# Optimization experiments

Measured on AMD Instinct MI355X. Metric: run time of the kernel, lower is better.

The kernel has to match this reference:

```python
import jax, jax.numpy as jnp
import numpy as np

N_PARTICLES = 100000
STATE_DIM = 64          # 3 + 2*2 + 57
MSG_OUT = 64
HIDDEN = 32
N_EDGES = 1600000


def _init_linear(key, fan_in, fan_out):
    kw, kb = jax.random.split(key)
    bound = 1.0 / np.sqrt(fan_in)
    W = jax.random.uniform(kw, (fan_in, fan_out), minval=-bound, maxval=bound, dtype=jnp.float32)
    b = jax.random.uniform(kb, (fan_out,), minval=-bound, maxval=bound, dtype=jnp.float32)
    return W, b


def setup_inputs() -> dict:
    key = jax.random.key(0)
    ks = jax.random.split(key, 8)
    x = jax.random.normal(ks[0], (N_PARTICLES, STATE_DIM), dtype=jnp.float32)
    edge_index = jax.random.randint(ks[1], (2, N_EDGES), 0, N_PARTICLES, dtype=jnp.int64)
    # message conv MLP: [2*STATE_DIM] -> 32 -> 32 -> MSG_OUT
    mW1, mb1 = _init_linear(ks[2], 2 * STATE_DIM, HIDDEN)
    mW2, mb2 = _init_linear(ks[3], HIDDEN, HIDDEN)
    mW3, mb3 = _init_linear(ks[4], HIDDEN, MSG_OUT)
    # own_state_nn MLP: [STATE_DIM + MSG_OUT] -> 32 -> 32 -> STATE_DIM
    oW1, ob1 = _init_linear(ks[5], STATE_DIM + MSG_OUT, HIDDEN)
    oW2, ob2 = _init_linear(ks[6], HIDDEN, HIDDEN)
    oW3, ob3 = _init_linear(ks[7], HIDDEN, STATE_DIM)
    return {"x": x, "edge_index": edge_index,
            "mW1": mW1, "mb1": mb1, "mW2": mW2, "mb2": mb2, "mW3": mW3, "mb3": mb3,
            "oW1": oW1, "ob1": ob1, "oW2": oW2, "ob2": ob2, "oW3": oW3, "ob3": ob3}


def _mlp3(h, W1, b1, W2, b2, W3, b3):
    h = jax.nn.relu(h @ W1 + b1)
    h = jax.nn.relu(h @ W2 + b2)
    return h @ W3 + b3


def reference(x, edge_index, mW1, mb1, mW2, mb2, mW3, mb3,
              oW1, ob1, oW2, ob2, oW3, ob3):
    src, dst = edge_index[0], edge_index[1]
    # edge-wise message: MLP over [x_src || x_dst]  -> [E, MSG_OUT]
    e_feat = jnp.concatenate([x[src], x[dst]], axis=-1)  # [E, 2*STATE_DIM]
    m = _mlp3(e_feat, mW1, mb1, mW2, mb2, mW3, mb3)
    # scatter-sum aggregation at destination node
    messages = jax.ops.segment_sum(m, dst, num_segments=x.shape[0])  # [N, MSG_OUT]
    combined = jnp.concatenate([x, messages], axis=-1)  # [N, STATE_DIM+MSG_OUT]
    new_state = _mlp3(combined, oW1, ob1, oW2, ob2, oW3, ob3)
    return new_state
```

## Files before the change

### kernel.cpp

```cpp
#include <hip/hip_runtime.h>

#define NP 100000
#define NE 1600000
#define SD 64
#define HID 32
#define MSG 64
#define NP_PAD 100352
#define NTILE (NP / 16)
#define BINSZ 512
#define NBIN ((NP + BINSZ - 1) / BINSZ)
#define EPW 8192
#define NWG ((NE + EPW - 1) / EPW)

typedef float v4f __attribute__((ext_vector_type(4)));
typedef short v4s __attribute__((ext_vector_type(4)));
typedef short v8s __attribute__((ext_vector_type(8)));
typedef __bf16 v8bf __attribute__((ext_vector_type(8)));

#define WQ_FRAGS 56

__device__ __forceinline__ v4f MFMA32(v8s a, v8s b, v4f c) {
  return __builtin_amdgcn_mfma_f32_16x16x32_bf16(
      __builtin_bit_cast(v8bf, a), __builtin_bit_cast(v8bf, b), c, 0, 0, 0);
}

__device__ __forceinline__ short f2bf(float f) {
  return __builtin_bit_cast(short, (__bf16)f);
}
__device__ __forceinline__ float bf2f(short s) {
  unsigned u = ((unsigned)(unsigned short)s) << 16;
  return __builtin_bit_cast(float, u);
}

__device__ __forceinline__ v4f mfma3(v8s ah, v8s al, v8s bh, v8s bl, v4f c) {
  c = MFMA32(al, bh, c);
  c = MFMA32(ah, bl, c);
  c = MFMA32(ah, bh, c);
  return c;
}

__device__ __forceinline__ void load_wfrag(const float* __restrict__ W, int ld,
                                           int kb, int m0, int lq, int l15,
                                           v8s* hi, v8s* lo) {
  v8s h, l;
#pragma unroll
  for (int j = 0; j < 8; ++j) {
    int k = kb + ((j < 4) ? (4 * lq + j) : (16 + 4 * lq + (j - 4)));
    float v = W[k * ld + m0 + l15];
    short hb = f2bf(v);
    h[j] = hb;
    l[j] = f2bf(v - bf2f(hb));
  }
  *hi = h;
  *lo = l;
}

__device__ __forceinline__ void split8(v4f a, v4f b, v8s* hi, v8s* lo) {
  v8s h, l;
#pragma unroll
  for (int j = 0; j < 4; ++j) {
    short ha = f2bf(a[j]); h[j] = ha; l[j] = f2bf(a[j] - bf2f(ha));
    short hb = f2bf(b[j]); h[j + 4] = hb; l[j + 4] = f2bf(b[j] - bf2f(hb));
  }
  *hi = h;
  *lo = l;
}

__device__ __forceinline__ void load_xfrag(const float* xs, int kb, int lq,
                                           v8s* hi, v8s* lo) {
  v4f a = *reinterpret_cast<const v4f*>(xs + kb + 4 * lq);
  v4f b = *reinterpret_cast<const v4f*>(xs + kb + 16 + 4 * lq);
  split8(a, b, hi, lo);
}

__device__ __forceinline__ void chain_frag(v4f d0, v4f d1, v8s* hi, v8s* lo) {
  v4f a, b;
#pragma unroll
  for (int j = 0; j < 4; ++j) {
    a[j] = fmaxf(d0[j], 0.f);
    b[j] = fmaxf(d1[j], 0.f);
  }
  split8(a, b, hi, lo);
}


__global__ void prew_kernel(const float* __restrict__ mW1,
                            const float* __restrict__ mW2,
                            const float* __restrict__ mW3,
                            const float* __restrict__ oW1,
                            const float* __restrict__ oW2,
                            const float* __restrict__ oW3,
                            short* __restrict__ wqs) {
  int lane = threadIdx.x;
  int l15 = lane & 15, lq = lane >> 4;
  v8s* wq = reinterpret_cast<v8s*>(wqs);
  v8s h, l;
#pragma unroll
  for (int t = 0; t < 2; ++t)
#pragma unroll
    for (int kc = 0; kc < 2; ++kc) {
      load_wfrag(mW1, HID, kc * 32, t * 16, lq, l15, &h, &l);
      wq[(t * 2 + kc) * 64 + lane] = h;
      wq[(4 + t * 2 + kc) * 64 + lane] = l;
      load_wfrag(mW1, HID, 64 + kc * 32, t * 16, lq, l15, &h, &l);
      wq[(8 + t * 2 + kc) * 64 + lane] = h;
      wq[(12 + t * 2 + kc) * 64 + lane] = l;
    }
#pragma unroll
  for (int t = 0; t < 2; ++t) {
    load_wfrag(mW2, HID, 0, t * 16, lq, l15, &h, &l);
    wq[(16 + t) * 64 + lane] = h;
    wq[(18 + t) * 64 + lane] = l;
  }
#pragma unroll
  for (int t = 0; t < 4; ++t) {
    load_wfrag(mW3, MSG, 0, t * 16, lq, l15, &h, &l);
    wq[(20 + t) * 64 + lane] = h;
    wq[(24 + t) * 64 + lane] = l;
  }
#pragma unroll
  for (int t = 0; t < 2; ++t)
#pragma unroll
    for (int kc = 0; kc < 4; ++kc) {
      load_wfrag(oW1, HID, kc * 32, t * 16, lq, l15, &h, &l);
      wq[(28 + t * 4 + kc) * 64 + lane] = h;
      wq[(36 + t * 4 + kc) * 64 + lane] = l;
    }
#pragma unroll
  for (int t = 0; t < 2; ++t) {
    load_wfrag(oW2, HID, 0, t * 16, lq, l15, &h, &l);
    wq[(44 + t) * 64 + lane] = h;
    wq[(46 + t) * 64 + lane] = l;
  }
#pragma unroll
  for (int t = 0; t < 4; ++t) {
    load_wfrag(oW3, SD, 0, t * 16, lq, l15, &h, &l);
    wq[(48 + t) * 64 + lane] = h;
    wq[(52 + t) * 64 + lane] = l;
  }
}

__global__ __launch_bounds__(256, 2) void prep_kernel(
    const float* __restrict__ x, const short* __restrict__ wqs,
    const float* __restrict__ mb1,
    float* __restrict__ h1d_buf, short* __restrict__ h1s_buf) {
  const int lane = threadIdx.x & 63;
  const int l15 = lane & 15;
  const int lq = lane >> 4;
  const int tile = (blockIdx.x * 256 + threadIdx.x) >> 6;
  if (tile >= NTILE) return;
  const v8s* wq = reinterpret_cast<const v8s*>(wqs);

  const int node = tile * 16 + l15;
  v4f d0, d1, s0 = {0.f, 0.f, 0.f, 0.f}, s1 = {0.f, 0.f, 0.f, 0.f};
#pragma unroll
  for (int q = 0; q < 4; ++q) {
    d0[q] = mb1[4 * lq + q];
    d1[q] = mb1[16 + 4 * lq + q];
  }
#pragma unroll
  for (int kc = 0; kc < 2; ++kc) {
    v8s xh, xl;
    load_xfrag(x + (size_t)node * SD, kc * 32, lq, &xh, &xl);
    d0 = mfma3(wq[(8 + kc) * 64 + lane], wq[(12 + kc) * 64 + lane], xh, xl, d0);
    d1 = mfma3(wq[(10 + kc) * 64 + lane], wq[(14 + kc) * 64 + lane], xh, xl, d1);
    s0 = mfma3(wq[(0 + kc) * 64 + lane], wq[(4 + kc) * 64 + lane], xh, xl, s0);
    s1 = mfma3(wq[(2 + kc) * 64 + lane], wq[(6 + kc) * 64 + lane], xh, xl, s1);
  }
  *reinterpret_cast<v4f*>(h1d_buf + (size_t)node * HID + 4 * lq) = d0;
  *reinterpret_cast<v4f*>(h1d_buf + (size_t)node * HID + 16 + 4 * lq) = d1;
  v4s q0, q1;
#pragma unroll
  for (int q = 0; q < 4; ++q) {
    q0[q] = f2bf(s0[q]);
    q1[q] = f2bf(s1[q]);
  }
  *reinterpret_cast<v4s*>(h1s_buf + (size_t)node * HID + 4 * lq) = q0;
  *reinterpret_cast<v4s*>(h1s_buf + (size_t)node * HID + 16 + 4 * lq) = q1;
}


__global__ __launch_bounds__(256) void bin_count_kernel(
    const int* __restrict__ ei, int* __restrict__ gOff) {
  __shared__ int cnt[NBIN];
  const int w = blockIdx.x;
  for (int i = threadIdx.x; i < NBIN; i += 256) cnt[i] = 0;
  __syncthreads();
  const int e0 = w * EPW;
  const int e1 = (e0 + EPW < NE) ? e0 + EPW : NE;
  for (int e = e0 + threadIdx.x; e < e1; e += 256)
    atomicAdd(&cnt[ei[NE + e] >> 9], 1);
  __syncthreads();
  for (int i = threadIdx.x; i < NBIN; i += 256) gOff[i * NWG + w] = cnt[i];
}

__global__ __launch_bounds__(256) void scan_bins_kernel(
    int* __restrict__ gOff, int* __restrict__ binStart) {
  __shared__ int tot[NBIN];
  const int b = threadIdx.x;
  if (b < NBIN) {
    int run = 0;
    for (int w = 0; w < NWG; ++w) {
      int v = gOff[b * NWG + w];
      gOff[b * NWG + w] = run;
      run += v;
    }
    tot[b] = run;
  }
  __syncthreads();
  if (threadIdx.x == 0) {
    int run = 0;
    for (int bb = 0; bb < NBIN; ++bb) {
      binStart[bb] = run;
      run += tot[bb];
    }
    binStart[NBIN] = run;
  }
  __syncthreads();
  if (b < NBIN) {
    int base = binStart[b];
    for (int w = 0; w < NWG; ++w) gOff[b * NWG + w] += base;
  }
}

__global__ __launch_bounds__(256) void bin_scatter_kernel(
    const int* __restrict__ ei, const int* __restrict__ gOff,
    int2* __restrict__ pairs) {
  __shared__ int cur[NBIN];
  const int w = blockIdx.x;
  for (int i = threadIdx.x; i < NBIN; i += 256) cur[i] = gOff[i * NWG + w];
  __syncthreads();
  const int e0 = w * EPW;
  const int e1 = (e0 + EPW < NE) ? e0 + EPW : NE;
  for (int e = e0 + threadIdx.x; e < e1; e += 256) {
    int s = ei[e];
    int d = ei[NE + e];
    int pos = atomicAdd(&cur[d >> 9], 1);
    pairs[pos] = make_int2(s, d);
  }
}

__global__ __launch_bounds__(512) void bin_csr_kernel(
    const int2* __restrict__ pairs, const int* __restrict__ binStart,
    int2* __restrict__ co, int* __restrict__ csr_src) {
  __shared__ int sh[BINSZ];
  __shared__ int cu[BINSZ];
  const int b = blockIdx.x;
  const int t = threadIdx.x;
  cu[t] = 0;
  __syncthreads();
  const int p0 = binStart[b], p1 = binStart[b + 1];
  for (int p = p0 + t; p < p1; p += BINSZ)
    atomicAdd(&cu[pairs[p].y & (BINSZ - 1)], 1);
  __syncthreads();
  const int v = cu[t];
  sh[t] = v;
  __syncthreads();
  for (int off = 1; off < BINSZ; off <<= 1) {
    int a = (t >= off) ? sh[t - off] : 0;
    __syncthreads();
    sh[t] += a;
    __syncthreads();
  }
  const int excl = sh[t] - v;
  const int node = b * BINSZ + t;
  if (node < NP) co[node] = make_int2(p0 + excl, v);
  cu[t] = excl;
  __syncthreads();
  for (int p = p0 + t; p < p1; p += BINSZ) {
    int2 pr = pairs[p];
    int loc = atomicAdd(&cu[pr.y & (BINSZ - 1)], 1);
    csr_src[p0 + loc] = pr.x;
  }
}

__global__ __launch_bounds__(256, 4) void edge_mfma_kernel(
    const short* __restrict__ h1s, const float* __restrict__ h1d_buf,
    const short* __restrict__ wqs, const int2* __restrict__ co,
    const int* __restrict__ csr_src, const float* __restrict__ mb2,
    float* __restrict__ rsum) {
  const int lane = threadIdx.x & 63;
  const int l15 = lane & 15;
  const int lq = lane >> 4;
  const int wid = (blockIdx.x * 256 + threadIdx.x) >> 6;
  const int nw = gridDim.x * 4;
  const v8s* wq = reinterpret_cast<const v8s*>(wqs);

  const v8s w2h0 = wq[16 * 64 + lane], w2h1 = wq[17 * 64 + lane];
  const v8s w2l0 = wq[18 * 64 + lane], w2l1 = wq[19 * 64 + lane];
  v4f bb0, bb1;
#pragma unroll
  for (int q = 0; q < 4; ++q) {
    bb0[q] = mb2[4 * lq + q];
    bb1[q] = mb2[16 + 4 * lq + q];
  }

  for (int n = wid; n < NP; n += nw) {
    const int2 c = co[n];
    const int off = c.x, cnt = c.y;
    const int ng = (cnt + 15) >> 4;

    const v4f h1d0 = *reinterpret_cast<const v4f*>(h1d_buf + (size_t)n * HID + 4 * lq);
    const v4f h1d1 = *reinterpret_cast<const v4f*>(h1d_buf + (size_t)n * HID + 16 + 4 * lq);

    v4f r0 = {0.f, 0.f, 0.f, 0.f}, r1 = {0.f, 0.f, 0.f, 0.f};

    int rem = cnt;
    bool vcur = l15 < rem;
    int scur = vcur ? csr_src[off + l15] : 0;
    v4s ca = *reinterpret_cast<const v4s*>(h1s + (size_t)scur * HID + 4 * lq);
    v4s cb = *reinterpret_cast<const v4s*>(h1s + (size_t)scur * HID + 16 + 4 * lq);

    for (int g = 0; g < ng; ++g) {
      int rem2 = rem - 16;
      bool vnxt = l15 < rem2;
      int snxt = vnxt ? csr_src[off + (g + 1) * 16 + l15] : 0;
      v4s na = *reinterpret_cast<const v4s*>(h1s + (size_t)snxt * HID + 4 * lq);
      v4s nb = *reinterpret_cast<const v4s*>(h1s + (size_t)snxt * HID + 16 + 4 * lq);

      v4f d0, d1;
#pragma unroll
      for (int q = 0; q < 4; ++q) {
        d0[q] = h1d0[q] + bf2f(ca[q]);
        d1[q] = h1d1[q] + bf2f(cb[q]);
      }

      v8s ph, pl;
      chain_frag(d0, d1, &ph, &pl);
      v4f e0 = bb0, e1 = bb1;
      e0 = mfma3(w2h0, w2l0, ph, pl, e0);
      e1 = mfma3(w2h1, w2l1, ph, pl, e1);

      if (vcur) {
#pragma unroll
        for (int j = 0; j < 4; ++j) {
          r0[j] += fmaxf(e0[j], 0.f);
          r1[j] += fmaxf(e1[j], 0.f);
        }
      }
      ca = na;
      cb = nb;
      vcur = vnxt;
      rem = rem2;
    }

#pragma unroll
    for (int j = 0; j < 4; ++j) {
      float a = r0[j], b = r1[j];
      a += __shfl_xor(a, 1); a += __shfl_xor(a, 2);
      a += __shfl_xor(a, 4); a += __shfl_xor(a, 8);
      b += __shfl_xor(b, 1); b += __shfl_xor(b, 2);
      b += __shfl_xor(b, 4); b += __shfl_xor(b, 8);
      r0[j] = a; r1[j] = b;
    }
    if (l15 == 0) {
      *reinterpret_cast<v4f*>(rsum + (size_t)n * HID + 4 * lq) = r0;
      *reinterpret_cast<v4f*>(rsum + (size_t)n * HID + 16 + 4 * lq) = r1;
    }
  }
}

__global__ __launch_bounds__(256, 2) void fused_tail_kernel(
    const float* __restrict__ x, const short* __restrict__ wqs,
    const float* __restrict__ rsum, const int2* __restrict__ co,
    const float* __restrict__ mb3,
    const float* __restrict__ ob1, const float* __restrict__ ob2,
    const float* __restrict__ ob3,
    float* __restrict__ out) {
  const int lane = threadIdx.x & 63;
  const int l15 = lane & 15;
  const int lq = lane >> 4;
  const int tile = (blockIdx.x * 256 + threadIdx.x) >> 6;
  if (tile >= NTILE) return;
  const v8s* wq = reinterpret_cast<const v8s*>(wqs);

  const int node = tile * 16 + l15;
  const float fc = (float)co[node].y;

  v4f ra = *reinterpret_cast<const v4f*>(rsum + (size_t)node * HID + 4 * lq);
  v4f rb = *reinterpret_cast<const v4f*>(rsum + (size_t)node * HID + 16 + 4 * lq);
  v8s bh, bl;
  split8(ra, rb, &bh, &bl);

  v4f m[4];
#pragma unroll
  for (int t = 0; t < 4; ++t) {
    v4f c = {0.f, 0.f, 0.f, 0.f};
    c = mfma3(wq[(20 + t) * 64 + lane], wq[(24 + t) * 64 + lane], bh, bl, c);
#pragma unroll
    for (int q = 0; q < 4; ++q) c[q] += fc * mb3[t * 16 + 4 * lq + q];
    m[t] = c;
  }

  v4f d0, d1;
#pragma unroll
  for (int q = 0; q < 4; ++q) {
    d0[q] = ob1[4 * lq + q];
    d1[q] = ob1[16 + 4 * lq + q];
  }
#pragma unroll
  for (int kc = 0; kc < 2; ++kc) {
    v8s xh, xl;
    load_xfrag(x + (size_t)node * SD, kc * 32, lq, &xh, &xl);
    d0 = mfma3(wq[(28 + kc) * 64 + lane], wq[(36 + kc) * 64 + lane], xh, xl, d0);
    d1 = mfma3(wq[(32 + kc) * 64 + lane], wq[(40 + kc) * 64 + lane], xh, xl, d1);
  }
#pragma unroll
  for (int kc = 0; kc < 2; ++kc) {
    v8s mh, ml;
    split8(m[kc * 2], m[kc * 2 + 1], &mh, &ml);
    d0 = mfma3(wq[(30 + kc) * 64 + lane], wq[(38 + kc) * 64 + lane], mh, ml, d0);
    d1 = mfma3(wq[(34 + kc) * 64 + lane], wq[(42 + kc) * 64 + lane], mh, ml, d1);
  }

  v8s ph, pl;
  chain_frag(d0, d1, &ph, &pl);
  v4f e0, e1;
#pragma unroll
  for (int q = 0; q < 4; ++q) {
    e0[q] = ob2[4 * lq + q];
    e1[q] = ob2[16 + 4 * lq + q];
  }
  e0 = mfma3(wq[44 * 64 + lane], wq[46 * 64 + lane], ph, pl, e0);
  e1 = mfma3(wq[45 * 64 + lane], wq[47 * 64 + lane], ph, pl, e1);

  v8s rh, rl;
  chain_frag(e0, e1, &rh, &rl);
  float* orow = out + (size_t)node * SD;
#pragma unroll
  for (int t = 0; t < 4; ++t) {
    v4f c;
#pragma unroll
    for (int q = 0; q < 4; ++q) c[q] = ob3[t * 16 + 4 * lq + q];
    c = mfma3(wq[(48 + t) * 64 + lane], wq[(52 + t) * 64 + lane], rh, rl, c);
    *reinterpret_cast<v4f*>(orow + t * 16 + 4 * lq) = c;
  }
}

extern "C" void kernel_launch(void* const* d_in, const int* in_sizes, int n_in,
                              void* d_out, int out_size, void* d_ws,
                              size_t ws_size, hipStream_t stream) {
  const float* x = (const float*)d_in[0];
  const int* ei = (const int*)d_in[1];
  const float* mW1 = (const float*)d_in[2];
  const float* mb1 = (const float*)d_in[3];
  const float* mW2 = (const float*)d_in[4];
  const float* mb2 = (const float*)d_in[5];
  const float* mW3 = (const float*)d_in[6];
  const float* mb3 = (const float*)d_in[7];
  const float* oW1 = (const float*)d_in[8];
  const float* ob1 = (const float*)d_in[9];
  const float* oW2 = (const float*)d_in[10];
  const float* ob2 = (const float*)d_in[11];
  const float* oW3 = (const float*)d_in[12];
  const float* ob3 = (const float*)d_in[13];
  float* out = (float*)d_out;

  float* h1d_buf = (float*)d_out;
  short* h1s_buf = (short*)((char*)d_out + (size_t)NP * HID * 4);

  char* p = (char*)d_ws;
  short* wqs = (short*)p;            p += (size_t)WQ_FRAGS * 64 * 16;
  int* gOff = (int*)p;               p += (size_t)NBIN * NWG * 4;
  int* binStart = (int*)p;           p += 200 * 4;
  int2* co = (int2*)p;               p += (size_t)NP_PAD * 8;
  int* csr_src = (int*)p;            p += (size_t)NE * 4;
  int2* pairs = (int2*)p;
  float* rsum = (float*)pairs;

  prew_kernel<<<1, 64, 0, stream>>>(mW1, mW2, mW3, oW1, oW2, oW3, wqs);

  const int tile_blocks = (NTILE + 3) / 4;
  prep_kernel<<<tile_blocks, 256, 0, stream>>>(x, wqs, mb1, h1d_buf, h1s_buf);

  bin_count_kernel<<<NWG, 256, 0, stream>>>(ei, gOff);
  scan_bins_kernel<<<1, 256, 0, stream>>>(gOff, binStart);
  bin_scatter_kernel<<<NWG, 256, 0, stream>>>(ei, gOff, pairs);
  bin_csr_kernel<<<NBIN, 512, 0, stream>>>(pairs, binStart, co, csr_src);

  edge_mfma_kernel<<<2048, 256, 0, stream>>>(
      h1s_buf, h1d_buf, wqs, co, csr_src, mb2, rsum);

  fused_tail_kernel<<<tile_blocks, 256, 0, stream>>>(
      x, wqs, rsum, co, mb3, ob1, ob2, ob3, out);
}
```

Measured before the change: 173.4 us.

## Merge weight prep, node prep and bin count into one launch; deepen edge prefetch

Three small kernels (weight fragment packing, per-node first-layer precompute, destination bin counting) become one setup kernel whose blocks pick a role from blockIdx. This removes two launches and their serialization gaps. The node-prep blocks now read and split mW1 fragments directly instead of waiting on packed weights. Separately, the edge loop prefetches source features two groups ahead instead of one, to hide more gather latency at the cost of extra registers.

```diff
diff --git a/kernel.cpp b/kernel.cpp
--- a/kernel.cpp
+++ b/kernel.cpp
@@ -7,6 +7,7 @@
 #define MSG 64
 #define NP_PAD 100352
 #define NTILE (NP / 16)
+#define TILE_BLOCKS ((NTILE + 3) / 4)
 #define BINSZ 512
 #define NBIN ((NP + BINSZ - 1) / BINSZ)
 #define EPW 8192
@@ -83,75 +84,87 @@
   split8(a, b, hi, lo);
 }
 
-
-__global__ void prew_kernel(const float* __restrict__ mW1,
-                            const float* __restrict__ mW2,
-                            const float* __restrict__ mW3,
-                            const float* __restrict__ oW1,
-                            const float* __restrict__ oW2,
-                            const float* __restrict__ oW3,
-                            short* __restrict__ wqs) {
-  int lane = threadIdx.x;
-  int l15 = lane & 15, lq = lane >> 4;
-  v8s* wq = reinterpret_cast<v8s*>(wqs);
-  v8s h, l;
-#pragma unroll
-  for (int t = 0; t < 2; ++t)
-#pragma unroll
-    for (int kc = 0; kc < 2; ++kc) {
-      load_wfrag(mW1, HID, kc * 32, t * 16, lq, l15, &h, &l);
-      wq[(t * 2 + kc) * 64 + lane] = h;
-      wq[(4 + t * 2 + kc) * 64 + lane] = l;
-      load_wfrag(mW1, HID, 64 + kc * 32, t * 16, lq, l15, &h, &l);
-      wq[(8 + t * 2 + kc) * 64 + lane] = h;
-      wq[(12 + t * 2 + kc) * 64 + lane] = l;
-    }
-#pragma unroll
-  for (int t = 0; t < 2; ++t) {
-    load_wfrag(mW2, HID, 0, t * 16, lq, l15, &h, &l);
-    wq[(16 + t) * 64 + lane] = h;
-    wq[(18 + t) * 64 + lane] = l;
-  }
-#pragma unroll
-  for (int t = 0; t < 4; ++t) {
-    load_wfrag(mW3, MSG, 0, t * 16, lq, l15, &h, &l);
-    wq[(20 + t) * 64 + lane] = h;
-    wq[(24 + t) * 64 + lane] = l;
-  }
-#pragma unroll
-  for (int t = 0; t < 2; ++t)
-#pragma unroll
-    for (int kc = 0; kc < 4; ++kc) {
-      load_wfrag(oW1, HID, kc * 32, t * 16, lq, l15, &h, &l);
-      wq[(28 + t * 4 + kc) * 64 + lane] = h;
-      wq[(36 + t * 4 + kc) * 64 + lane] = l;
-    }
-#pragma unroll
-  for (int t = 0; t < 2; ++t) {
-    load_wfrag(oW2, HID, 0, t * 16, lq, l15, &h, &l);
-    wq[(44 + t) * 64 + lane] = h;
-    wq[(46 + t) * 64 + lane] = l;
-  }
-#pragma unroll
-  for (int t = 0; t < 4; ++t) {
-    load_wfrag(oW3, SD, 0, t * 16, lq, l15, &h, &l);
-    wq[(48 + t) * 64 + lane] = h;
-    wq[(52 + t) * 64 + lane] = l;
-  }
-}
-
-__global__ __launch_bounds__(256, 2) void prep_kernel(
-    const float* __restrict__ x, const short* __restrict__ wqs,
-    const float* __restrict__ mb1,
+__global__ __launch_bounds__(256, 2) void setup_kernel(
+    const float* __restrict__ x, const int* __restrict__ ei,
+    const float* __restrict__ mW1, const float* __restrict__ mb1,
+    const float* __restrict__ mW2, const float* __restrict__ mW3,
+    const float* __restrict__ oW1, const float* __restrict__ oW2,
+    const float* __restrict__ oW3,
+    int* __restrict__ gOff, short* __restrict__ wqs,
     float* __restrict__ h1d_buf, short* __restrict__ h1s_buf) {
+  __shared__ int cnt[NBIN];
+  const int blk = blockIdx.x;
+
+  if (blk < NWG) {
+    for (int i = threadIdx.x; i < NBIN; i += 256) cnt[i] = 0;
+    __syncthreads();
+    const int e0 = blk * EPW;
+    const int e1 = (e0 + EPW < NE) ? e0 + EPW : NE;
+    for (int e = e0 + threadIdx.x; e < e1; e += 256)
+      atomicAdd(&cnt[ei[NE + e] >> 9], 1);
+    __syncthreads();
+    for (int i = threadIdx.x; i < NBIN; i += 256) gOff[i * NWG + blk] = cnt[i];
+    return;
+  }
+
   const int lane = threadIdx.x & 63;
   const int l15 = lane & 15;
   const int lq = lane >> 4;
-  const int tile = (blockIdx.x * 256 + threadIdx.x) >> 6;
+
+  if (blk == NWG) {
+    if (threadIdx.x >= 64) return;
+    v8s* wq = reinterpret_cast<v8s*>(wqs);
+    v8s h, l;
+#pragma unroll
+    for (int t = 0; t < 2; ++t)
+#pragma unroll
+      for (int kc = 0; kc < 2; ++kc) {
+        load_wfrag(mW1, HID, kc * 32, t * 16, lq, l15, &h, &l);
+        wq[(t * 2 + kc) * 64 + lane] = h;
+        wq[(4 + t * 2 + kc) * 64 + lane] = l;
+        load_wfrag(mW1, HID, 64 + kc * 32, t * 16, lq, l15, &h, &l);
+        wq[(8 + t * 2 + kc) * 64 + lane] = h;
+        wq[(12 + t * 2 + kc) * 64 + lane] = l;
+      }
+#pragma unroll
+    for (int t = 0; t < 2; ++t) {
+      load_wfrag(mW2, HID, 0, t * 16, lq, l15, &h, &l);
+      wq[(16 + t) * 64 + lane] = h;
+      wq[(18 + t) * 64 + lane] = l;
+    }
+#pragma unroll
+    for (int t = 0; t < 4; ++t) {
+      load_wfrag(mW3, MSG, 0, t * 16, lq, l15, &h, &l);
+      wq[(20 + t) * 64 + lane] = h;
+      wq[(24 + t) * 64 + lane] = l;
+    }
+#pragma unroll
+    for (int t = 0; t < 2; ++t)
+#pragma unroll
+      for (int kc = 0; kc < 4; ++kc) {
+        load_wfrag(oW1, HID, kc * 32, t * 16, lq, l15, &h, &l);
+        wq[(28 + t * 4 + kc) * 64 + lane] = h;
+        wq[(36 + t * 4 + kc) * 64 + lane] = l;
+      }
+#pragma unroll
+    for (int t = 0; t < 2; ++t) {
+      load_wfrag(oW2, HID, 0, t * 16, lq, l15, &h, &l);
+      wq[(44 + t) * 64 + lane] = h;
+      wq[(46 + t) * 64 + lane] = l;
+    }
+#pragma unroll
+    for (int t = 0; t < 4; ++t) {
+      load_wfrag(oW3, SD, 0, t * 16, lq, l15, &h, &l);
+      wq[(48 + t) * 64 + lane] = h;
+      wq[(52 + t) * 64 + lane] = l;
+    }
+    return;
+  }
+
+  const int tile = ((blk - NWG - 1) * 256 + (int)threadIdx.x) >> 6;
   if (tile >= NTILE) return;
-  const v8s* wq = reinterpret_cast<const v8s*>(wqs);
-
   const int node = tile * 16 + l15;
+
   v4f d0, d1, s0 = {0.f, 0.f, 0.f, 0.f}, s1 = {0.f, 0.f, 0.f, 0.f};
 #pragma unroll
   for (int q = 0; q < 4; ++q) {
@@ -160,12 +173,16 @@
   }
 #pragma unroll
   for (int kc = 0; kc < 2; ++kc) {
-    v8s xh, xl;
+    v8s xh, xl, wh, wl;
     load_xfrag(x + (size_t)node * SD, kc * 32, lq, &xh, &xl);
-    d0 = mfma3(wq[(8 + kc) * 64 + lane], wq[(12 + kc) * 64 + lane], xh, xl, d0);
-    d1 = mfma3(wq[(10 + kc) * 64 + lane], wq[(14 + kc) * 64 + lane], xh, xl, d1);
-    s0 = mfma3(wq[(0 + kc) * 64 + lane], wq[(4 + kc) * 64 + lane], xh, xl, s0);
-    s1 = mfma3(wq[(2 + kc) * 64 + lane], wq[(6 + kc) * 64 + lane], xh, xl, s1);
+    load_wfrag(mW1, HID, 64 + kc * 32, 0, lq, l15, &wh, &wl);
+    d0 = mfma3(wh, wl, xh, xl, d0);
+    load_wfrag(mW1, HID, 64 + kc * 32, 16, lq, l15, &wh, &wl);
+    d1 = mfma3(wh, wl, xh, xl, d1);
+    load_wfrag(mW1, HID, kc * 32, 0, lq, l15, &wh, &wl);
+    s0 = mfma3(wh, wl, xh, xl, s0);
+    load_wfrag(mW1, HID, kc * 32, 16, lq, l15, &wh, &wl);
+    s1 = mfma3(wh, wl, xh, xl, s1);
   }
   *reinterpret_cast<v4f*>(h1d_buf + (size_t)node * HID + 4 * lq) = d0;
   *reinterpret_cast<v4f*>(h1d_buf + (size_t)node * HID + 16 + 4 * lq) = d1;
@@ -179,20 +196,6 @@
   *reinterpret_cast<v4s*>(h1s_buf + (size_t)node * HID + 16 + 4 * lq) = q1;
 }
 
-
-__global__ __launch_bounds__(256) void bin_count_kernel(
-    const int* __restrict__ ei, int* __restrict__ gOff) {
-  __shared__ int cnt[NBIN];
-  const int w = blockIdx.x;
-  for (int i = threadIdx.x; i < NBIN; i += 256) cnt[i] = 0;
-  __syncthreads();
-  const int e0 = w * EPW;
-  const int e1 = (e0 + EPW < NE) ? e0 + EPW : NE;
-  for (int e = e0 + threadIdx.x; e < e1; e += 256)
-    atomicAdd(&cnt[ei[NE + e] >> 9], 1);
-  __syncthreads();
-  for (int i = threadIdx.x; i < NBIN; i += 256) gOff[i * NWG + w] = cnt[i];
-}
 
 __global__ __launch_bounds__(256) void scan_bins_kernel(
     int* __restrict__ gOff, int* __restrict__ binStart) {
@@ -305,24 +308,22 @@
 
     v4f r0 = {0.f, 0.f, 0.f, 0.f}, r1 = {0.f, 0.f, 0.f, 0.f};
 
+    int sa = (l15 < cnt) ? csr_src[off + l15] : 0;
+    v4s a0 = *reinterpret_cast<const v4s*>(h1s + (size_t)sa * HID + 4 * lq);
+    v4s b0 = *reinterpret_cast<const v4s*>(h1s + (size_t)sa * HID + 16 + 4 * lq);
+    int sb = (l15 < cnt - 16) ? csr_src[off + 16 + l15] : 0;
+    v4s a1 = *reinterpret_cast<const v4s*>(h1s + (size_t)sb * HID + 4 * lq);
+    v4s b1 = *reinterpret_cast<const v4s*>(h1s + (size_t)sb * HID + 16 + 4 * lq);
+
     int rem = cnt;
-    bool vcur = l15 < rem;
-    int scur = vcur ? csr_src[off + l15] : 0;
-    v4s ca = *reinterpret_cast<const v4s*>(h1s + (size_t)scur * HID + 4 * lq);
-    v4s cb = *reinterpret_cast<const v4s*>(h1s + (size_t)scur * HID + 16 + 4 * lq);
-
     for (int g = 0; g < ng; ++g) {
-      int rem2 = rem - 16;
-      bool vnxt = l15 < rem2;
-      int snxt = vnxt ? csr_src[off + (g + 1) * 16 + l15] : 0;
-      v4s na = *reinterpret_cast<const v4s*>(h1s + (size_t)snxt * HID + 4 * lq);
-      v4s nb = *reinterpret_cast<const v4s*>(h1s + (size_t)snxt * HID + 16 + 4 * lq);
+      int sc = (l15 < rem - 32) ? csr_src[off + (g + 2) * 16 + l15] : 0;
 
       v4f d0, d1;
 #pragma unroll
       for (int q = 0; q < 4; ++q) {
-        d0[q] = h1d0[q] + bf2f(ca[q]);
-        d1[q] = h1d1[q] + bf2f(cb[q]);
+        d0[q] = h1d0[q] + bf2f(a0[q]);
+        d1[q] = h1d1[q] + bf2f(b0[q]);
       }
 
       v8s ph, pl;
@@ -331,17 +332,20 @@
       e0 = mfma3(w2h0, w2l0, ph, pl, e0);
       e1 = mfma3(w2h1, w2l1, ph, pl, e1);
 
-      if (vcur) {
+      if (l15 < rem) {
 #pragma unroll
         for (int j = 0; j < 4; ++j) {
           r0[j] += fmaxf(e0[j], 0.f);
           r1[j] += fmaxf(e1[j], 0.f);
         }
       }
-      ca = na;
-      cb = nb;
-      vcur = vnxt;
-      rem = rem2;
+
+      v4s a2 = *reinterpret_cast<const v4s*>(h1s + (size_t)sc * HID + 4 * lq);
+      v4s b2 = *reinterpret_cast<const v4s*>(h1s + (size_t)sc * HID + 16 + 4 * lq);
+
+      a0 = a1; b0 = b1;
+      a1 = a2; b1 = b2;
+      rem -= 16;
     }
 
 #pragma unroll
@@ -468,12 +472,9 @@
   int2* pairs = (int2*)p;
   float* rsum = (float*)pairs;
 
-  prew_kernel<<<1, 64, 0, stream>>>(mW1, mW2, mW3, oW1, oW2, oW3, wqs);
-
-  const int tile_blocks = (NTILE + 3) / 4;
-  prep_kernel<<<tile_blocks, 256, 0, stream>>>(x, wqs, mb1, h1d_buf, h1s_buf);
-
-  bin_count_kernel<<<NWG, 256, 0, stream>>>(ei, gOff);
+  setup_kernel<<<NWG + 1 + TILE_BLOCKS, 256, 0, stream>>>(
+      x, ei, mW1, mb1, mW2, mW3, oW1, oW2, oW3, gOff, wqs, h1d_buf, h1s_buf);
+
   scan_bins_kernel<<<1, 256, 0, stream>>>(gOff, binStart);
   bin_scatter_kernel<<<NWG, 256, 0, stream>>>(ei, gOff, pairs);
   bin_csr_kernel<<<NBIN, 512, 0, stream>>>(pairs, binStart, co, csr_src);
@@ -481,6 +482,6 @@
   edge_mfma_kernel<<<2048, 256, 0, stream>>>(
       h1s_buf, h1d_buf, wqs, co, csr_src, mb2, rsum);
 
-  fused_tail_kernel<<<tile_blocks, 256, 0, stream>>>(
+  fused_tail_kernel<<<TILE_BLOCKS, 256, 0, stream>>>(
       x, wqs, rsum, co, mb3, ob1, ob2, ob3, out);
 }
```

Measured after the change: 158.1 us. 1.1x faster.
